# Performance work log

Hardware: AMD Instinct MI355X
Metric: run time of the kernel (lower is better)

Reference implementation:

```python
import jax
jax.config.update("jax_enable_x64", True)
import jax.numpy as jnp
import numpy as np
import math

B, L = 4, 4096
VOCAB, CVOCAB = 32000, 25000
HIDDEN, EDIM, NHEADS = 1024, 64, 8
NGRAMS = (2, 3)
TABLE_HINT = 100003
KSIZE, DILATION = 4, 3  # dilation = max ngram order
EPS = 1e-6


def _next_prime(n):
    if n <= 2:
        return 2
    c = n if n % 2 else n + 1
    while True:
        if all(c % i for i in range(3, int(math.isqrt(c)) + 1, 2)):
            return c
        c += 2


def _table_sizes():
    sizes, cur = [], TABLE_HINT
    for _ in range(NHEADS):
        p = _next_prime(cur)
        sizes.append(p)
        cur = p + 2
    return sizes


def setup_inputs():
    key = jax.random.key(0)
    ks = jax.random.split(key, 12)
    sizes = _table_sizes()  # identical for both ngram orders (same hint)
    max_s = max(sizes)
    n_orders = NGRAMS[1] - NGRAMS[0] + 1  # 2
    table_sizes = jnp.asarray(np.tile(np.array(sizes, dtype=np.int64), (n_orders, 1)))  # [2,8]
    tables = 0.01 * jax.random.normal(ks[0], (n_orders, NHEADS, max_s, EDIM), dtype=jnp.float32)
    return {
        "hidden_states": jax.random.normal(ks[1], (B, L, HIDDEN), dtype=jnp.float32),
        "token_ids": jax.random.randint(ks[2], (B, L), 0, VOCAB, dtype=jnp.int64),
        "projection": jax.random.randint(ks[3], (VOCAB,), 0, CVOCAB, dtype=jnp.int64),
        "mults2": jax.random.randint(ks[4], (NHEADS, 2), 1, 2**31 - 1, dtype=jnp.int64),
        "mults3": jax.random.randint(ks[5], (NHEADS, 3), 1, 2**31 - 1, dtype=jnp.int64),
        "table_sizes": table_sizes,
        "tables": tables,
        "w_k": (jax.random.normal(ks[6], (HIDDEN, n_orders * NHEADS * EDIM), dtype=jnp.float32) / math.sqrt(n_orders * NHEADS * EDIM)),
        "w_v": (jax.random.normal(ks[7], (HIDDEN, n_orders * NHEADS * EDIM), dtype=jnp.float32) / math.sqrt(n_orders * NHEADS * EDIM)),
        "q_norm_w": jnp.ones((HIDDEN,), dtype=jnp.float32),
        "k_norm_w": jnp.ones((HIDDEN,), dtype=jnp.float32),
        "conv_norm_w": jnp.ones((HIDDEN,), dtype=jnp.float32),
        "conv_w": 0.02 * jax.random.normal(ks[8], (HIDDEN, KSIZE), dtype=jnp.float32),
        "conv_b": jnp.zeros((HIDDEN,), dtype=jnp.float32),
    }


def _rmsnorm(x, w):
    norm = jax.lax.rsqrt(jnp.mean(jnp.square(x.astype(jnp.float32)), axis=-1, keepdims=True) + EPS)
    return (x.astype(jnp.float32) * norm).astype(x.dtype) * w


def _build_ngrams(compressed, n):
    # compressed: [B,L] int64 -> [B,L,n] causal windows with left zero pad
    p = jnp.pad(compressed, ((0, 0), (n - 1, 0)))
    return jnp.stack([p[:, i:i + compressed.shape[1]] for i in range(n)], axis=-1)


def _hash(ngrams, mults, sizes):
    # ngrams [B,L,n], mults [H,n], sizes [H] -> [B,L,H]
    prod = ngrams[:, :, None, :] * mults[None, None, :, :]  # int64
    mix = prod[..., 0]
    for i in range(1, prod.shape[-1]):
        mix = mix ^ prod[..., i]
    return jnp.abs(mix) % sizes[None, None, :]


def reference(hidden_states, token_ids, projection, mults2, mults3, table_sizes,
              tables, w_k, w_v, q_norm_w, k_norm_w, conv_norm_w, conv_w, conv_b):
    b, l, hidden = hidden_states.shape
    # ---- retrieve ----
    compressed = projection[jnp.clip(token_ids, 0, projection.shape[0] - 1)]  # [B,L]
    idx2 = _hash(_build_ngrams(compressed, 2), mults2, table_sizes[0])  # [B,L,H]
    idx3 = _hash(_build_ngrams(compressed, 3), mults3, table_sizes[1])  # [B,L,H]
    idx = jnp.concatenate([idx2, idx3], axis=-1)  # [B,L,2H] order: ngram2 heads, ngram3 heads
    n_tab = tables.shape[0] * tables.shape[1]
    tab_flat = tables.reshape(n_tab, tables.shape[2], tables.shape[3])
    emb = tab_flat[jnp.arange(n_tab), idx]  # [B,L,2H,EDIM] gather
    memory = emb.reshape(b, l, -1)  # [B,L,total_retrieval_dim]
    # ---- fuse ----
    k = jnp.einsum('bld,hd->blh', memory, w_k)
    v = jnp.einsum('bld,hd->blh', memory, w_v)
    q_n = _rmsnorm(hidden_states, q_norm_w)
    k_n = _rmsnorm(k, k_norm_w)
    scale = 1.0 / math.sqrt(hidden)
    gate = jax.nn.sigmoid(jnp.sum(q_n * k_n, axis=-1, keepdims=True) * scale)
    v_g = gate * v
    # ---- short conv (causal depthwise, dilation=3, kernel=4) ----
    h = _rmsnorm(v_g, conv_norm_w)
    pad = (KSIZE - 1) * DILATION  # 9; right padding is sliced off by [..., :L]
    hp = jnp.pad(h, ((0, 0), (pad, 0), (0, 0)))
    y = conv_b
    for j in range(KSIZE):
        y = y + hp[:, j * DILATION: j * DILATION + l, :] * conv_w[None, None, :, j]
    return jax.nn.silu(y) + v_g


if __name__ == "__main__":
    out = reference(**setup_inputs())
    print(out.shape, out.dtype)
```

## Files before the change

### kernel.cpp

```cpp
#include <hip/hip_runtime.h>
#include <hip/hip_bf16.h>
#include <math.h>

typedef unsigned short u16;
typedef __bf16 bf16x8 __attribute__((ext_vector_type(8)));
typedef float f32x4 __attribute__((ext_vector_type(4)));
typedef unsigned short u16x4 __attribute__((ext_vector_type(4)));

#define BB 4
#define LL 4096
#define MTOK (BB*LL)
#define HID 1024
#define RD 1024
#define NKV 2048
#define KDIM 1024
#define VOCABN 32000
#define EPSF 1e-6f

__device__ __forceinline__ float bf2f(u16 x) {
  unsigned u = ((unsigned)x) << 16;
  return __builtin_bit_cast(float, u);
}
__device__ __forceinline__ u16 f2bf(float f) {
  unsigned u = __builtin_bit_cast(unsigned, f);
  u += 0x7FFFu + ((u >> 16) & 1u);
  return (u16)(u >> 16);
}

__global__ __launch_bounds__(256) void k_convert_w(const float* __restrict__ wk,
                                                   const float* __restrict__ wv,
                                                   u16* __restrict__ W) {
  int i = blockIdx.x * 256 + threadIdx.x;
  const int n4 = (NKV * KDIM) / 4;
  if (i >= n4) return;
  const int half = n4 / 2;
  const f32x4* src = (i < half) ? (const f32x4*)wk : (const f32x4*)wv;
  int j = (i < half) ? i : i - half;
  f32x4 v = src[j];
  u16x4 o = { f2bf(v[0]), f2bf(v[1]), f2bf(v[2]), f2bf(v[3]) };
  *(u16x4*)&W[(size_t)i * 4] = o;
}

__global__ __launch_bounds__(256) void k_gather(
    const int* __restrict__ tok, const int* __restrict__ proj,
    const int* __restrict__ m2, const int* __restrict__ m3,
    const int* __restrict__ tsz, const float* __restrict__ tables,
    int max_s, u16* __restrict__ mem) {
  int m = blockIdx.x;
  int l = m & (LL - 1);
  int tid = threadIdx.x;
  int t = tid >> 4;
  int q = tid & 15;
  long long c0, c1 = 0, c2 = 0;
  {
    int tk = tok[m];
    tk = tk < 0 ? 0 : (tk > VOCABN - 1 ? VOCABN - 1 : tk);
    c0 = proj[tk];
  }
  if (l >= 1) {
    int tk = tok[m - 1];
    tk = tk < 0 ? 0 : (tk > VOCABN - 1 ? VOCABN - 1 : tk);
    c1 = proj[tk];
  }
  if (l >= 2) {
    int tk = tok[m - 2];
    tk = tk < 0 ? 0 : (tk > VOCABN - 1 ? VOCABN - 1 : tk);
    c2 = proj[tk];
  }
  int order = t >> 3, h = t & 7;
  long long mix;
  if (order == 0) {
    mix = (c1 * (long long)m2[h * 2 + 0]) ^ (c0 * (long long)m2[h * 2 + 1]);
  } else {
    mix = (c2 * (long long)m3[h * 3 + 0]) ^ (c1 * (long long)m3[h * 3 + 1]) ^
          (c0 * (long long)m3[h * 3 + 2]);
  }
  unsigned long long um = (unsigned long long)(mix < 0 ? -mix : mix);
  unsigned long long usz = (unsigned long long)tsz[t];
  unsigned long long qq = (unsigned long long)((double)um / (double)usz);
  long long r = (long long)(um - qq * usz);
  if (r < 0) r += (long long)usz;
  else if (r >= (long long)usz) r -= (long long)usz;
  const f32x4* src = (const f32x4*)(tables + ((size_t)t * (size_t)max_s + (size_t)r) * 64);
  f32x4 e = src[q];
  u16x4 o = { f2bf(e[0]), f2bf(e[1]), f2bf(e[2]), f2bf(e[3]) };
  *(u16x4*)&mem[(size_t)m * RD + t * 64 + q * 4] = o;
}

#define GBK2 32
#define NT2 32
#define BUF2 32768

__device__ __forceinline__ void gload16(const void* g, void* l) {
  __builtin_amdgcn_global_load_lds((__attribute__((address_space(1))) void*)(g),
                                   (__attribute__((address_space(3))) void*)(l), 16, 0, 0);
}
__device__ __forceinline__ int swz32(int x) { return x ^ (((x >> 6) & 3) << 4); }

__global__ __launch_bounds__(512, 2) void k_gemm(const u16* __restrict__ A,
                                                 const u16* __restrict__ Bw,
                                                 u16* __restrict__ C) {
  __shared__ __align__(16) char lds[131072];
  const int d = blockIdx.x;
  const int wg = (d & 7) * 64 + (d >> 3);
  const int bm = wg >> 3, bn = wg & 7;
  const int tid = threadIdx.x;
  const int w = tid >> 6, lane = tid & 63;
  const int wm = w >> 2, wn = w & 3;
  const int lm = lane & 15, kg = lane >> 4;

  const int ca0 = w * 2, ca1 = w * 2 + 1;
  const int row0 = ca0 * 16 + (lane >> 2);
  const int row1 = ca1 * 16 + (lane >> 2);
  const int off0 = row0 * KDIM + (((lane & 3) ^ (row0 & 3)) << 3);
  const int off1 = row1 * KDIM + (((lane & 3) ^ (row1 & 3)) << 3);
  const int dstA0 = ca0 * 1024 + lane * 16;
  const int dstA1 = ca1 * 1024 + lane * 16;
  const u16* Ap = A + (size_t)bm * 256 * KDIM;
  const u16* Bp = Bw + (size_t)bn * 256 * KDIM;

  int aro[8], bro[4];
#pragma unroll
  for (int mi = 0; mi < 8; ++mi)
    aro[mi] = swz32((wm * 128 + mi * 16 + lm) * 64 + kg * 16);
#pragma unroll
  for (int ni = 0; ni < 4; ++ni)
    bro[ni] = 16384 + swz32((wn * 64 + ni * 16 + lm) * 64 + kg * 16);

  f32x4 acc[8][4];
#pragma unroll
  for (int i = 0; i < 8; ++i)
#pragma unroll
    for (int j = 0; j < 4; ++j) acc[i][j] = (f32x4){0.f, 0.f, 0.f, 0.f};

#define STG(kt, bb)                                                        \
  {                                                                        \
    char* bbase = lds + (bb) * BUF2;                                       \
    gload16(Ap + off0 + (kt) * GBK2, bbase + dstA0);                       \
    gload16(Bp + off0 + (kt) * GBK2, bbase + 16384 + dstA0);               \
    gload16(Ap + off1 + (kt) * GBK2, bbase + dstA1);                       \
    gload16(Bp + off1 + (kt) * GBK2, bbase + 16384 + dstA1);               \
  }

#define TILE(t, bb, VMS, DOSTG)                                            \
  {                                                                        \
    asm volatile("s_waitcnt vmcnt(" VMS ")" ::: "memory");                 \
    __builtin_amdgcn_s_barrier();                                          \
    if (DOSTG) STG((t) + 2, ((bb) + 2) & 3);                               \
    const char* buf = lds + (bb) * BUF2;                                   \
    bf16x8 af[8], bf[4];                                                   \
    _Pragma("unroll")                                                      \
    for (int mi = 0; mi < 8; ++mi) af[mi] = *(const bf16x8*)(buf + aro[mi]); \
    _Pragma("unroll")                                                      \
    for (int ni = 0; ni < 4; ++ni) bf[ni] = *(const bf16x8*)(buf + bro[ni]); \
    asm volatile("s_waitcnt lgkmcnt(0)" ::: "memory");                     \
    __builtin_amdgcn_sched_barrier(0);                                     \
    __builtin_amdgcn_s_setprio(1);                                         \
    _Pragma("unroll")                                                      \
    for (int mi = 0; mi < 8; ++mi)                                         \
      _Pragma("unroll")                                                    \
      for (int ni = 0; ni < 4; ++ni)                                       \
        acc[mi][ni] = __builtin_amdgcn_mfma_f32_16x16x32_bf16(af[mi], bf[ni], acc[mi][ni], 0, 0, 0); \
    __builtin_amdgcn_s_setprio(0);                                         \
  }

  STG(0, 0);
  STG(1, 1);
#pragma unroll 1
  for (int t4 = 0; t4 < 7; ++t4) {
    const int t = t4 * 4;
    TILE(t + 0, 0, "4", 1);
    TILE(t + 1, 1, "4", 1);
    TILE(t + 2, 2, "4", 1);
    TILE(t + 3, 3, "4", 1);
  }
  TILE(28, 0, "4", 1);
  TILE(29, 1, "4", 1);
  TILE(30, 2, "4", 0);
  TILE(31, 3, "0", 0);
#undef STG
#undef TILE

  __syncthreads();
  u16* tile = (u16*)lds;
#pragma unroll
  for (int mi = 0; mi < 8; ++mi)
#pragma unroll
    for (int ni = 0; ni < 4; ++ni)
#pragma unroll
      for (int jj = 0; jj < 4; ++jj) {
        int r = wm * 128 + mi * 16 + kg * 4 + jj;
        int ccol = wn * 64 + ni * 16 + lm;
        tile[r * 256 + ccol] = f2bf(acc[mi][ni][jj]);
      }
  __syncthreads();
#pragma unroll
  for (int it = 0; it < 8; ++it) {
    int r = it * 32 + (tid >> 4);
    int cb = (tid & 15) * 32;
    *(f32x4*)((char*)C + ((size_t)(bm * 256 + r) * NKV + bn * 256) * 2 + cb) =
        *(const f32x4*)((char*)tile + r * 512 + cb);
    *(f32x4*)((char*)C + ((size_t)(bm * 256 + r) * NKV + bn * 256) * 2 + cb + 16) =
        *(const f32x4*)((char*)tile + r * 512 + cb + 16);
  }
}

#define CR 32

__global__ __launch_bounds__(256) void k_gateconv(
    const float* __restrict__ hidden, const u16* __restrict__ KV,
    const float* __restrict__ qw, const float* __restrict__ kw,
    const float* __restrict__ cw, const float* __restrict__ convw,
    const float* __restrict__ convb, float* __restrict__ out) {
  __shared__ float ring[10][1024];
  __shared__ float red[4][4];
  const int blk = blockIdx.x;
  const int b = blk >> 7;
  const int l0 = (blk & 127) * CR;
  const int tid = threadIdx.x;
  const int c = tid * 4;
  const int w = tid >> 6, ln = tid & 63;

  f32x4 qv = *(const f32x4*)&qw[c];
  f32x4 kv = *(const f32x4*)&kw[c];
  f32x4 cwv = *(const f32x4*)&cw[c];
  f32x4 cb = *(const f32x4*)&convb[c];
  f32x4 wt0 = *(const f32x4*)&convw[c * 4];
  f32x4 wt1 = *(const f32x4*)&convw[(c + 1) * 4];
  f32x4 wt2 = *(const f32x4*)&convw[(c + 2) * 4];
  f32x4 wt3 = *(const f32x4*)&convw[(c + 3) * 4];

  int slot = 0;
  f32x4 px = (f32x4){0.f, 0.f, 0.f, 0.f};
  u16x4 pk = (u16x4){0, 0, 0, 0}, pv = (u16x4){0, 0, 0, 0};
  if (l0 - 9 >= 0) {
    size_t m = (size_t)b * LL + (l0 - 9);
    px = *(const f32x4*)&hidden[m * HID + c];
    pk = *(const u16x4*)&KV[m * NKV + c];
    pv = *(const u16x4*)&KV[m * NKV + HID + c];
  }

  for (int r = l0 - 9; r < l0 + CR; ++r) {
    const bool live = (r >= 0);
    f32x4 x = px;
    u16x4 kk = pk, vvx = pv;
    if (r + 1 < l0 + CR && r + 1 >= 0) {
      size_t m2 = (size_t)b * LL + (r + 1);
      px = *(const f32x4*)&hidden[m2 * HID + c];
      pk = *(const u16x4*)&KV[m2 * NKV + c];
      pv = *(const u16x4*)&KV[m2 * NKV + HID + c];
    }
    float s0 = 0.f, s1 = 0.f, s2 = 0.f, s3 = 0.f;
    float kf[4], vf[4];
    if (live) {
#pragma unroll
      for (int i = 0; i < 4; ++i) {
        kf[i] = bf2f(kk[i]);
        vf[i] = bf2f(vvx[i]);
        s0 += x[i] * x[i];
        s1 += kf[i] * kf[i];
        s2 += (x[i] * qv[i]) * (kf[i] * kv[i]);
        s3 += vf[i] * vf[i];
      }
    }
#pragma unroll
    for (int mm = 32; mm >= 1; mm >>= 1) {
      s0 += __shfl_xor(s0, mm, 64);
      s1 += __shfl_xor(s1, mm, 64);
      s2 += __shfl_xor(s2, mm, 64);
      s3 += __shfl_xor(s3, mm, 64);
    }
    __syncthreads();
    if (ln == 0) { red[w][0] = s0; red[w][1] = s1; red[w][2] = s2; red[w][3] = s3; }
    __syncthreads();
    float t0 = red[0][0] + red[1][0] + red[2][0] + red[3][0];
    float t1 = red[0][1] + red[1][1] + red[2][1] + red[3][1];
    float t2 = red[0][2] + red[1][2] + red[2][2] + red[3][2];
    float t3 = red[0][3] + red[1][3] + red[2][3] + red[3][3];

    f32x4 vg = (f32x4){0.f, 0.f, 0.f, 0.f};
    float h[4] = {0.f, 0.f, 0.f, 0.f};
    if (live) {
      const float inv = 0.0009765625f;
      float rq = rsqrtf(t0 * inv + EPSF);
      float rk = rsqrtf(t1 * inv + EPSF);
      float gate = 1.f / (1.f + expf(-rq * rk * t2 * 0.03125f));
      float rv = rsqrtf(gate * gate * t3 * inv + EPSF);
      float grv = gate * rv;
#pragma unroll
      for (int i = 0; i < 4; ++i) {
        vg[i] = gate * vf[i];
        h[i] = vf[i] * grv * cwv[i];
      }
    }
    *(f32x4*)&ring[slot][c] = (f32x4){h[0], h[1], h[2], h[3]};

    if (r >= l0) {
      int s9 = slot + 1; s9 = s9 >= 10 ? s9 - 10 : s9;
      int s6 = slot + 4; s6 = s6 >= 10 ? s6 - 10 : s6;
      int s3v = slot + 7; s3v = s3v >= 10 ? s3v - 10 : s3v;
      f32x4 h9 = *(const f32x4*)&ring[s9][c];
      f32x4 h6 = *(const f32x4*)&ring[s6][c];
      f32x4 h3 = *(const f32x4*)&ring[s3v][c];
      f32x4 res;
#pragma unroll
      for (int i = 0; i < 4; ++i) {
        f32x4 wt = (i == 0) ? wt0 : (i == 1) ? wt1 : (i == 2) ? wt2 : wt3;
        float y = cb[i] + h9[i] * wt[0] + h6[i] * wt[1] + h3[i] * wt[2] + h[i] * wt[3];
        res[i] = y / (1.f + expf(-y)) + vg[i];
      }
      *(f32x4*)&out[((size_t)b * LL + r) * HID + c] = res;
    }
    slot = slot + 1 >= 10 ? 0 : slot + 1;
  }
}

extern "C" void kernel_launch(void* const* d_in, const int* in_sizes, int n_in,
                              void* d_out, int out_size, void* d_ws, size_t ws_size,
                              hipStream_t stream) {
  const float* hidden   = (const float*)d_in[0];
  const int*   tok      = (const int*)d_in[1];
  const int*   proj     = (const int*)d_in[2];
  const int*   m2       = (const int*)d_in[3];
  const int*   m3       = (const int*)d_in[4];
  const int*   tsz      = (const int*)d_in[5];
  const float* tables   = (const float*)d_in[6];
  const float* wk       = (const float*)d_in[7];
  const float* wv       = (const float*)d_in[8];
  const float* qw       = (const float*)d_in[9];
  const float* kw       = (const float*)d_in[10];
  const float* cnw      = (const float*)d_in[11];
  const float* convw    = (const float*)d_in[12];
  const float* convb    = (const float*)d_in[13];
  float* out = (float*)d_out;

  const int max_s = in_sizes[6] / (2 * 8 * 64);

  char* ws = (char*)d_ws;
  u16* mem = (u16*)ws;
  u16* W   = (u16*)(ws + (size_t)33554432);
  u16* KV  = (u16*)(ws + (size_t)33554432 + 4194304);

  k_convert_w<<<dim3((NKV * KDIM / 4 + 255) / 256), dim3(256), 0, stream>>>(wk, wv, W);
  k_gather<<<dim3(MTOK), dim3(256), 0, stream>>>(tok, proj, m2, m3, tsz, tables, max_s, mem);
  k_gemm<<<dim3((MTOK / 256) * (NKV / 256)), dim3(512), 0, stream>>>(mem, W, KV);
  k_gateconv<<<dim3(BB * (LL / CR)), dim3(256), 0, stream>>>(hidden, KV, qw, kw, cnw, convw, convb, out);
}
```

Measured before the change: 182.3 us.

## Deepen GEMM prefetch to three stages and restructure gate-conv to wave-per-row

The GEMM pipeline now keeps three K-tiles in flight instead of two, using the fourth LDS buffer and waiting on vmcnt 8. The gate/conv kernel is rewritten so that each wavefront handles a whole row (1024 channels, 16 per lane). Row reductions then use only wave shuffles, without the LDS reduction and extra barrier, and four rows are processed per iteration with a single barrier. The conv history ring is stored as bf16 in a 32-slot LDS buffer, which adds rounding of the normalized intermediate and raises register pressure under the two-blocks-per-SM launch bound.

```diff
diff --git a/kernel.cpp b/kernel.cpp
--- a/kernel.cpp
+++ b/kernel.cpp
@@ -6,12 +6,12 @@
 typedef __bf16 bf16x8 __attribute__((ext_vector_type(8)));
 typedef float f32x4 __attribute__((ext_vector_type(4)));
 typedef unsigned short u16x4 __attribute__((ext_vector_type(4)));
+typedef unsigned short u16x8 __attribute__((ext_vector_type(8)));
 
 #define BB 4
 #define LL 4096
 #define MTOK (BB*LL)
 #define HID 1024
-#define RD 1024
 #define NKV 2048
 #define KDIM 1024
 #define VOCABN 32000
@@ -84,11 +84,10 @@
   const f32x4* src = (const f32x4*)(tables + ((size_t)t * (size_t)max_s + (size_t)r) * 64);
   f32x4 e = src[q];
   u16x4 o = { f2bf(e[0]), f2bf(e[1]), f2bf(e[2]), f2bf(e[3]) };
-  *(u16x4*)&mem[(size_t)m * RD + t * 64 + q * 4] = o;
+  *(u16x4*)&mem[(size_t)m * HID + t * 64 + q * 4] = o;
 }
 
 #define GBK2 32
-#define NT2 32
 #define BUF2 32768
 
 __device__ __forceinline__ void gload16(const void* g, void* l) {
@@ -146,7 +145,7 @@
   {                                                                        \
     asm volatile("s_waitcnt vmcnt(" VMS ")" ::: "memory");                 \
     __builtin_amdgcn_s_barrier();                                          \
-    if (DOSTG) STG((t) + 2, ((bb) + 2) & 3);                               \
+    if (DOSTG) STG((t) + 3, ((bb) + 3) & 3);                               \
     const char* buf = lds + (bb) * BUF2;                                   \
     bf16x8 af[8], bf[4];                                                   \
     _Pragma("unroll")                                                      \
@@ -166,16 +165,17 @@
 
   STG(0, 0);
   STG(1, 1);
+  STG(2, 2);
 #pragma unroll 1
   for (int t4 = 0; t4 < 7; ++t4) {
     const int t = t4 * 4;
-    TILE(t + 0, 0, "4", 1);
-    TILE(t + 1, 1, "4", 1);
-    TILE(t + 2, 2, "4", 1);
-    TILE(t + 3, 3, "4", 1);
-  }
-  TILE(28, 0, "4", 1);
-  TILE(29, 1, "4", 1);
+    TILE(t + 0, 0, "8", 1);
+    TILE(t + 1, 1, "8", 1);
+    TILE(t + 2, 2, "8", 1);
+    TILE(t + 3, 3, "8", 1);
+  }
+  TILE(28, 0, "8", 1);
+  TILE(29, 1, "8", 0);
   TILE(30, 2, "4", 0);
   TILE(31, 3, "0", 0);
 #undef STG
@@ -207,61 +207,79 @@
 
 #define CR 32
 
-__global__ __launch_bounds__(256) void k_gateconv(
+__global__ __launch_bounds__(256, 2) void k_gateconv(
     const float* __restrict__ hidden, const u16* __restrict__ KV,
     const float* __restrict__ qw, const float* __restrict__ kw,
     const float* __restrict__ cw, const float* __restrict__ convw,
     const float* __restrict__ convb, float* __restrict__ out) {
-  __shared__ float ring[10][1024];
-  __shared__ float red[4][4];
+  __shared__ u16 ring[32][1024];
   const int blk = blockIdx.x;
   const int b = blk >> 7;
   const int l0 = (blk & 127) * CR;
-  const int tid = threadIdx.x;
-  const int c = tid * 4;
-  const int w = tid >> 6, ln = tid & 63;
-
-  f32x4 qv = *(const f32x4*)&qw[c];
-  f32x4 kv = *(const f32x4*)&kw[c];
-  f32x4 cwv = *(const f32x4*)&cw[c];
-  f32x4 cb = *(const f32x4*)&convb[c];
-  f32x4 wt0 = *(const f32x4*)&convw[c * 4];
-  f32x4 wt1 = *(const f32x4*)&convw[(c + 1) * 4];
-  f32x4 wt2 = *(const f32x4*)&convw[(c + 2) * 4];
-  f32x4 wt3 = *(const f32x4*)&convw[(c + 3) * 4];
-
-  int slot = 0;
-  f32x4 px = (f32x4){0.f, 0.f, 0.f, 0.f};
-  u16x4 pk = (u16x4){0, 0, 0, 0}, pv = (u16x4){0, 0, 0, 0};
-  if (l0 - 9 >= 0) {
-    size_t m = (size_t)b * LL + (l0 - 9);
-    px = *(const f32x4*)&hidden[m * HID + c];
-    pk = *(const u16x4*)&KV[m * NKV + c];
-    pv = *(const u16x4*)&KV[m * NKV + HID + c];
-  }
-
-  for (int r = l0 - 9; r < l0 + CR; ++r) {
-    const bool live = (r >= 0);
-    f32x4 x = px;
-    u16x4 kk = pk, vvx = pv;
-    if (r + 1 < l0 + CR && r + 1 >= 0) {
-      size_t m2 = (size_t)b * LL + (r + 1);
-      px = *(const f32x4*)&hidden[m2 * HID + c];
-      pk = *(const u16x4*)&KV[m2 * NKV + c];
-      pv = *(const u16x4*)&KV[m2 * NKV + HID + c];
+  const int w = threadIdx.x >> 6, ln = threadIdx.x & 63;
+
+  float qk[16], cwv[16];
+  f32x4 wt[16];
+  f32x4 cbv[4];
+#pragma unroll
+  for (int seg = 0; seg < 2; ++seg) {
+    int c0 = seg * 512 + ln * 8;
+    f32x4 qa = *(const f32x4*)&qw[c0], qb = *(const f32x4*)&qw[c0 + 4];
+    f32x4 ka = *(const f32x4*)&kw[c0], kb = *(const f32x4*)&kw[c0 + 4];
+    f32x4 ca = *(const f32x4*)&cw[c0], cbx = *(const f32x4*)&cw[c0 + 4];
+#pragma unroll
+    for (int i = 0; i < 4; ++i) {
+      qk[seg * 8 + i] = qa[i] * ka[i];
+      qk[seg * 8 + 4 + i] = qb[i] * kb[i];
+      cwv[seg * 8 + i] = ca[i];
+      cwv[seg * 8 + 4 + i] = cbx[i];
+    }
+    cbv[seg * 2] = *(const f32x4*)&convb[c0];
+    cbv[seg * 2 + 1] = *(const f32x4*)&convb[c0 + 4];
+#pragma unroll
+    for (int e = 0; e < 8; ++e) wt[seg * 8 + e] = *(const f32x4*)&convw[(c0 + e) * 4];
+  }
+
+  const int base = l0 - 12;
+  f32x4 x0, x1, x2, x3, nx0, nx1, nx2, nx3;
+  u16x8 kk0, kk1, vv0, vv1, nk0, nk1, nv0, nv1;
+
+#define LOADROW(r, X0, X1, X2, X3, K0, K1, V0, V1)                             \
+  {                                                                            \
+    X0 = (f32x4){0.f,0.f,0.f,0.f}; X1 = X0; X2 = X0; X3 = X0;                  \
+    K0 = (u16x8){0,0,0,0,0,0,0,0}; K1 = K0; V0 = K0; V1 = K0;                  \
+    if ((r) >= l0 - 9 && (r) >= 0) {                                           \
+      size_t mr = (size_t)b * LL + (r);                                        \
+      X0 = *(const f32x4*)&hidden[mr * HID + ln * 8];                          \
+      X1 = *(const f32x4*)&hidden[mr * HID + ln * 8 + 4];                      \
+      X2 = *(const f32x4*)&hidden[mr * HID + 512 + ln * 8];                    \
+      X3 = *(const f32x4*)&hidden[mr * HID + 512 + ln * 8 + 4];                \
+      K0 = *(const u16x8*)&KV[mr * NKV + ln * 8];                              \
+      K1 = *(const u16x8*)&KV[mr * NKV + 512 + ln * 8];                        \
+      V0 = *(const u16x8*)&KV[mr * NKV + HID + ln * 8];                        \
+      V1 = *(const u16x8*)&KV[mr * NKV + HID + 512 + ln * 8];                  \
+    }                                                                          \
+  }
+
+  LOADROW(base + w, x0, x1, x2, x3, kk0, kk1, vv0, vv1);
+
+#pragma unroll 1
+  for (int g = 0; g < 11; ++g) {
+    const int r = base + g * 4 + w;
+    if (g < 10) {
+      LOADROW(r + 4, nx0, nx1, nx2, nx3, nk0, nk1, nv0, nv1);
     }
     float s0 = 0.f, s1 = 0.f, s2 = 0.f, s3 = 0.f;
-    float kf[4], vf[4];
-    if (live) {
-#pragma unroll
-      for (int i = 0; i < 4; ++i) {
-        kf[i] = bf2f(kk[i]);
-        vf[i] = bf2f(vvx[i]);
-        s0 += x[i] * x[i];
-        s1 += kf[i] * kf[i];
-        s2 += (x[i] * qv[i]) * (kf[i] * kv[i]);
-        s3 += vf[i] * vf[i];
-      }
+#pragma unroll
+    for (int e = 0; e < 8; ++e) {
+      float xa = (e < 4) ? x0[e] : x1[e - 4];
+      float xb = (e < 4) ? x2[e] : x3[e - 4];
+      float ka = bf2f(kk0[e]), kb = bf2f(kk1[e]);
+      float va = bf2f(vv0[e]), vb = bf2f(vv1[e]);
+      s0 += xa * xa + xb * xb;
+      s1 += ka * ka + kb * kb;
+      s2 += xa * qk[e] * ka + xb * qk[8 + e] * kb;
+      s3 += va * va + vb * vb;
     }
 #pragma unroll
     for (int mm = 32; mm >= 1; mm >>= 1) {
@@ -270,49 +288,53 @@
       s2 += __shfl_xor(s2, mm, 64);
       s3 += __shfl_xor(s3, mm, 64);
     }
+    const float inv = 0.0009765625f;
+    float rq = rsqrtf(s0 * inv + EPSF);
+    float rk = rsqrtf(s1 * inv + EPSF);
+    float gate = 1.f / (1.f + expf(-rq * rk * s2 * 0.03125f));
+    float rv = rsqrtf(gate * gate * s3 * inv + EPSF);
+    float grv = gate * rv;
+
+    u16x8 h0p, h1p;
+#pragma unroll
+    for (int e = 0; e < 8; ++e) {
+      h0p[e] = f2bf(bf2f(vv0[e]) * grv * cwv[e]);
+      h1p[e] = f2bf(bf2f(vv1[e]) * grv * cwv[8 + e]);
+    }
+    const int slot = r & 31;
+    *(u16x8*)&ring[slot][ln * 8] = h0p;
+    *(u16x8*)&ring[slot][512 + ln * 8] = h1p;
     __syncthreads();
-    if (ln == 0) { red[w][0] = s0; red[w][1] = s1; red[w][2] = s2; red[w][3] = s3; }
-    __syncthreads();
-    float t0 = red[0][0] + red[1][0] + red[2][0] + red[3][0];
-    float t1 = red[0][1] + red[1][1] + red[2][1] + red[3][1];
-    float t2 = red[0][2] + red[1][2] + red[2][2] + red[3][2];
-    float t3 = red[0][3] + red[1][3] + red[2][3] + red[3][3];
-
-    f32x4 vg = (f32x4){0.f, 0.f, 0.f, 0.f};
-    float h[4] = {0.f, 0.f, 0.f, 0.f};
-    if (live) {
-      const float inv = 0.0009765625f;
-      float rq = rsqrtf(t0 * inv + EPSF);
-      float rk = rsqrtf(t1 * inv + EPSF);
-      float gate = 1.f / (1.f + expf(-rq * rk * t2 * 0.03125f));
-      float rv = rsqrtf(gate * gate * t3 * inv + EPSF);
-      float grv = gate * rv;
-#pragma unroll
-      for (int i = 0; i < 4; ++i) {
-        vg[i] = gate * vf[i];
-        h[i] = vf[i] * grv * cwv[i];
+
+    if (r >= l0) {
+      const int s9 = (r - 9) & 31, s6 = (r - 6) & 31, s3s = (r - 3) & 31;
+      size_t mr = (size_t)b * LL + r;
+#pragma unroll
+      for (int seg = 0; seg < 2; ++seg) {
+        u16x8 a9 = *(const u16x8*)&ring[s9][seg * 512 + ln * 8];
+        u16x8 a6 = *(const u16x8*)&ring[s6][seg * 512 + ln * 8];
+        u16x8 a3 = *(const u16x8*)&ring[s3s][seg * 512 + ln * 8];
+        const u16x8 vv = seg ? vv1 : vv0;
+        f32x4 ra, rb;
+#pragma unroll
+        for (int e = 0; e < 8; ++e) {
+          const int idx = seg * 8 + e;
+          float vf = bf2f(vv[e]);
+          float hown = vf * grv * cwv[idx];
+          f32x4 wv = wt[idx];
+          float y = cbv[seg * 2 + (e >> 2)][e & 3] + bf2f(a9[e]) * wv[0] +
+                    bf2f(a6[e]) * wv[1] + bf2f(a3[e]) * wv[2] + hown * wv[3];
+          float res = y / (1.f + expf(-y)) + gate * vf;
+          if (e < 4) ra[e] = res; else rb[e - 4] = res;
+        }
+        *(f32x4*)&out[mr * HID + seg * 512 + ln * 8] = ra;
+        *(f32x4*)&out[mr * HID + seg * 512 + ln * 8 + 4] = rb;
       }
     }
-    *(f32x4*)&ring[slot][c] = (f32x4){h[0], h[1], h[2], h[3]};
-
-    if (r >= l0) {
-      int s9 = slot + 1; s9 = s9 >= 10 ? s9 - 10 : s9;
-      int s6 = slot + 4; s6 = s6 >= 10 ? s6 - 10 : s6;
-      int s3v = slot + 7; s3v = s3v >= 10 ? s3v - 10 : s3v;
-      f32x4 h9 = *(const f32x4*)&ring[s9][c];
-      f32x4 h6 = *(const f32x4*)&ring[s6][c];
-      f32x4 h3 = *(const f32x4*)&ring[s3v][c];
-      f32x4 res;
-#pragma unroll
-      for (int i = 0; i < 4; ++i) {
-        f32x4 wt = (i == 0) ? wt0 : (i == 1) ? wt1 : (i == 2) ? wt2 : wt3;
-        float y = cb[i] + h9[i] * wt[0] + h6[i] * wt[1] + h3[i] * wt[2] + h[i] * wt[3];
-        res[i] = y / (1.f + expf(-y)) + vg[i];
-      }
-      *(f32x4*)&out[((size_t)b * LL + r) * HID + c] = res;
-    }
-    slot = slot + 1 >= 10 ? 0 : slot + 1;
-  }
+    x0 = nx0; x1 = nx1; x2 = nx2; x3 = nx3;
+    kk0 = nk0; kk1 = nk1; vv0 = nv0; vv1 = nv1;
+  }
+#undef LOADROW
 }
 
 extern "C" void kernel_launch(void* const* d_in, const int* in_sizes, int n_in,
```

Measured after the change: 160.5 us. 12.0% less time.
